# Kernel optimization log

Hardware: AMD Instinct MI355X
Metric: run time of the kernel (lower is better)

Reference implementation:

```python
import jax, jax.numpy as jnp
import numpy as np

BALL_SIZE = 128


def setup_inputs() -> dict:
    key = jax.random.key(0)
    kq, kk, kv = jax.random.split(key, 3)
    B, H, n, Dh = 4, 16, 8192, 64
    q = jax.random.normal(kq, (B, H, n, Dh), dtype=jnp.float32)
    k = jax.random.normal(kk, (B, H, n, Dh), dtype=jnp.float32)
    v = jax.random.normal(kv, (B, H, n, Dh), dtype=jnp.float32)
    return {"q": q, "k": k, "v": v}


def reference(q, k, v) -> jnp.ndarray:
    # Block-local (ball) attention: attention computed independently within
    # each contiguous ball of size BALL_SIZE along the sequence dim.
    B, H, n, Dh = q.shape
    bs = BALL_SIZE
    m = n // bs
    # (B, H, m, bs, D) -- split seq into balls; attention only within a ball.
    qb = q.reshape(B, H, m, bs, Dh)
    kb = k.reshape(B, H, m, bs, Dh)
    vb = v.reshape(B, H, m, bs, Dh)
    scale = 1.0 / jnp.sqrt(jnp.asarray(Dh, dtype=q.dtype))
    scores = jnp.einsum('bhmqd,bhmkd->bhmqk', qb, kb) * scale  # (B,H,m,bs,bs)
    attn = jax.nn.softmax(scores, axis=-1)
    out = jnp.einsum('bhmqk,bhmkd->bhmqd', attn, vb)
    return out.reshape(B, H, n, Dh)
```

## Files before the change

kernel.cpp:

```cpp
#include <hip/hip_runtime.h>

typedef _Float16 half2_t __attribute__((ext_vector_type(2)));
typedef _Float16 half4_t __attribute__((ext_vector_type(4)));
typedef _Float16 half8_t __attribute__((ext_vector_type(8)));
typedef __fp16   fp16x2  __attribute__((ext_vector_type(2)));
typedef float    f32x16  __attribute__((ext_vector_type(16)));

#define BS 128
#define DH 64

static __device__ __forceinline__ half2_t pkrtz(float x, float y) {
  fp16x2 t = __builtin_amdgcn_cvt_pkrtz(x, y);
  return __builtin_bit_cast(half2_t, t);
}
static __device__ __forceinline__ unsigned pkrtz_u(float x, float y) {
  fp16x2 t = __builtin_amdgcn_cvt_pkrtz(x, y);
  return __builtin_bit_cast(unsigned, t);
}

static __device__ __forceinline__ half8_t cvt8(const float4 a, const float4 b) {
  half2_t h0 = pkrtz(a.x, a.y);
  half2_t h1 = pkrtz(a.z, a.w);
  half2_t h2 = pkrtz(b.x, b.y);
  half2_t h3 = pkrtz(b.z, b.w);
  half4_t lo = __builtin_shufflevector(h0, h1, 0, 1, 2, 3);
  half4_t hi = __builtin_shufflevector(h2, h3, 0, 1, 2, 3);
  return __builtin_shufflevector(lo, hi, 0, 1, 2, 3, 4, 5, 6, 7);
}

static __device__ __forceinline__ half8_t h8_from(unsigned r0, unsigned r1,
                                                  unsigned r2, unsigned r3) {
  half2_t h0 = __builtin_bit_cast(half2_t, r0);
  half2_t h1 = __builtin_bit_cast(half2_t, r1);
  half2_t h2 = __builtin_bit_cast(half2_t, r2);
  half2_t h3 = __builtin_bit_cast(half2_t, r3);
  half4_t lo = __builtin_shufflevector(h0, h1, 0, 1, 2, 3);
  half4_t hi = __builtin_shufflevector(h2, h3, 0, 1, 2, 3);
  return __builtin_shufflevector(lo, hi, 0, 1, 2, 3, 4, 5, 6, 7);
}

static __device__ __forceinline__ void plswap(unsigned x, unsigned y,
                                              unsigned& olo, unsigned& ohi) {
#if __has_builtin(__builtin_amdgcn_permlane32_swap)
  auto pr = __builtin_amdgcn_permlane32_swap((int)x, (int)y, false, false);
  unsigned tmp[2];
  __builtin_memcpy(tmp, &pr, 8);
  olo = tmp[0];
  ohi = tmp[1];
#else
  const int h = (threadIdx.x & 63) >> 5;
  unsigned xs = (unsigned)__shfl_xor((int)x, 32);
  unsigned ys = (unsigned)__shfl_xor((int)y, 32);
  olo = h ? ys : x;
  ohi = h ? y : xs;
#endif
}

static __device__ __forceinline__ int svt(int d) { return (d & 7) ^ ((d >> 2) & 7); }

__global__ __launch_bounds__(256) void ball_attn_kernel(
    const float* __restrict__ Q, const float* __restrict__ Kk,
    const float* __restrict__ V, float* __restrict__ O) {
  __shared__ __align__(16) float    Kf[BS * DH];
  __shared__ __align__(16) _Float16 VT[DH * BS];

  const int tid  = threadIdx.x;
  const int w    = tid >> 6;
  const int lane = tid & 63;
  const int ld   = lane & 31;
  const int hi   = lane >> 5;

  const int nwg  = gridDim.x;
  const int bid  = blockIdx.x;
  const int ball = (bid & 7) * (nwg >> 3) + (bid >> 3);

  const size_t base = (size_t)ball * (BS * DH);
  const float* Qb = Q + base;
  const float* Kb = Kk + base;
  const float* Vb = V + base;
  float*       Ob = O + base;

  const int kgrp = tid >> 4;
  const int d0   = (tid & 15) * 4;
  const int qbase = 32 * w;

#pragma unroll
  for (int t = 0; t < 8; ++t) {
    const int r = 32 * w + 4 * t + (lane >> 4);
    const int u = (lane & 15) ^ (r & 15);
    __builtin_amdgcn_global_load_lds(
        (const __attribute__((address_space(1))) unsigned int*)(Kb + r * DH + u * 4),
        (__attribute__((address_space(3))) unsigned int*)&Kf[(32 * w + 4 * t) * DH],
        16, 0, 0);
  }
  float4 va[4], vb[4];
#pragma unroll
  for (int it = 0; it < 4; ++it) {
    const int keyA = 2 * kgrp + 32 * it;
    va[it] = *(const float4*)(Vb + (size_t)keyA * DH + d0);
    vb[it] = *(const float4*)(Vb + (size_t)(keyA + 1) * DH + d0);
  }
  float4 qa[4], qb[4];
#pragma unroll
  for (int ds = 0; ds < 4; ++ds) {
    const float* qp = Qb + (qbase + ld) * DH + ds * 16 + hi * 8;
    qa[ds] = *(const float4*)qp;
    qb[ds] = *(const float4*)(qp + 4);
  }
#pragma unroll
  for (int it = 0; it < 4; ++it) {
    const int keyA = 2 * kgrp + 32 * it;
    const float* ap = (const float*)&va[it];
    const float* bp = (const float*)&vb[it];
#pragma unroll
    for (int j = 0; j < 4; ++j) {
      const int d = d0 + j;
      *(half2_t*)&VT[d * BS + (keyA ^ (svt(d) << 3))] = pkrtz(ap[j], bp[j]);
    }
  }
  half8_t bq[4];
#pragma unroll
  for (int ds = 0; ds < 4; ++ds) bq[ds] = cvt8(qa[ds], qb[ds]);

  __syncthreads();

  f32x16 acc[4] = {};
  __builtin_amdgcn_s_setprio(1);
#pragma unroll
  for (int kt = 0; kt < 4; ++kt) {
    const int row = kt * 32 + ld;
    const int sr  = row & 15;
    const float* kr = &Kf[row * DH];
#pragma unroll
    for (int ds = 0; ds < 4; ++ds) {
      const int u0 = 4 * ds + 2 * hi;
      const float4 a = *(const float4*)&kr[(u0 ^ sr) * 4];
      const float4 b = *(const float4*)&kr[((u0 + 1) ^ sr) * 4];
      const half8_t ak = cvt8(a, b);
      acc[kt] = __builtin_amdgcn_mfma_f32_32x32x16_f16(ak, bq[ds], acc[kt], 0, 0, 0);
    }
  }
  __builtin_amdgcn_s_setprio(0);

  float sm = 0.f;
#pragma unroll
  for (int kt = 0; kt < 4; ++kt)
#pragma unroll
    for (int r = 0; r < 16; ++r) {
      const float p = __expf(acc[kt][r] * 0.125f);
      acc[kt][r] = p;
      sm += p;
    }
  sm += __shfl_xor(sm, 32);
  const float inv = __builtin_amdgcn_rcpf(sm);

  half8_t pf[8];
#pragma unroll
  for (int s = 0; s < 8; ++s) {
    const int kt = s >> 1;
    const int bA = 2 * (s & 1);
    const int bB = bA + 1;
    const unsigned A0 = pkrtz_u(acc[kt][4 * bA + 0] * inv, acc[kt][4 * bA + 1] * inv);
    const unsigned A1 = pkrtz_u(acc[kt][4 * bA + 2] * inv, acc[kt][4 * bA + 3] * inv);
    const unsigned B0 = pkrtz_u(acc[kt][4 * bB + 0] * inv, acc[kt][4 * bB + 1] * inv);
    const unsigned B1 = pkrtz_u(acc[kt][4 * bB + 2] * inv, acc[kt][4 * bB + 3] * inv);
    unsigned r0, r1, r2, r3;
    plswap(A0, B0, r0, r2);
    plswap(A1, B1, r1, r3);
    pf[s] = h8_from(r0, r1, r2, r3);
  }

  f32x16 o[2] = {};
  __builtin_amdgcn_s_setprio(1);
#pragma unroll
  for (int dt = 0; dt < 2; ++dt) {
    const int row = dt * 32 + ld;
    const int sv  = svt(row) << 3;
#pragma unroll
    for (int s = 0; s < 8; ++s) {
      const half8_t vf = *(const half8_t*)&VT[row * BS + ((16 * s + 8 * hi) ^ sv)];
      o[dt] = __builtin_amdgcn_mfma_f32_32x32x16_f16(pf[s], vf, o[dt], 0, 0, 0);
    }
  }
  __builtin_amdgcn_s_setprio(0);

#pragma unroll
  for (int dt = 0; dt < 2; ++dt)
#pragma unroll
    for (int r = 0; r < 16; ++r) {
      const int qrow = qbase + (r & 3) + 8 * (r >> 2) + 4 * hi;
      Ob[qrow * DH + dt * 32 + ld] = o[dt][r];
    }
}

extern "C" void kernel_launch(void* const* d_in, const int* in_sizes, int n_in,
                              void* d_out, int out_size, void* d_ws, size_t ws_size,
                              hipStream_t stream) {
  const float* q = (const float*)d_in[0];
  const float* k = (const float*)d_in[1];
  const float* v = (const float*)d_in[2];
  float* out = (float*)d_out;
  const int nballs = in_sizes[0] / (BS * DH);
  ball_attn_kernel<<<dim3(nballs), dim3(256), 0, stream>>>(q, k, v, out);
}
```

Measured before the change: 111.6 us.

## Stage K as fp16 in LDS and process two balls per 512-thread block

K is now loaded into registers, converted to fp16 once, and stored to a swizzled fp16 LDS tile, so each wave reads ready-made half8 fragments. This replaces the asynchronous global-to-LDS fp32 copy followed by conversion after each LDS read. Each workgroup now handles two balls with 512 threads and double-sized shared arrays, halving the grid. The cost is losing the async global_load_lds path, more registers held per thread, and a different occupancy profile.

```diff
diff --git a/kernel.cpp b/kernel.cpp
--- a/kernel.cpp
+++ b/kernel.cpp
@@ -16,6 +16,12 @@
 static __device__ __forceinline__ unsigned pkrtz_u(float x, float y) {
   fp16x2 t = __builtin_amdgcn_cvt_pkrtz(x, y);
   return __builtin_bit_cast(unsigned, t);
+}
+
+static __device__ __forceinline__ half4_t cvt4(const float4 a) {
+  half2_t h0 = pkrtz(a.x, a.y);
+  half2_t h1 = pkrtz(a.z, a.w);
+  return __builtin_shufflevector(h0, h1, 0, 1, 2, 3);
 }
 
 static __device__ __forceinline__ half8_t cvt8(const float4 a, const float4 b) {
@@ -58,55 +64,64 @@
 
 static __device__ __forceinline__ int svt(int d) { return (d & 7) ^ ((d >> 2) & 7); }
 
-__global__ __launch_bounds__(256) void ball_attn_kernel(
+__global__ __launch_bounds__(512) void ball_attn_kernel(
     const float* __restrict__ Q, const float* __restrict__ Kk,
     const float* __restrict__ V, float* __restrict__ O) {
-  __shared__ __align__(16) float    Kf[BS * DH];
-  __shared__ __align__(16) _Float16 VT[DH * BS];
+  __shared__ __align__(16) _Float16 KH[2][BS * DH];
+  __shared__ __align__(16) _Float16 VT[2][DH * BS];
 
   const int tid  = threadIdx.x;
-  const int w    = tid >> 6;
+  const int w8   = tid >> 6;
+  const int grp  = w8 >> 2;
+  const int w    = w8 & 3;
   const int lane = tid & 63;
   const int ld   = lane & 31;
   const int hi   = lane >> 5;
-
-  const int nwg  = gridDim.x;
-  const int bid  = blockIdx.x;
-  const int ball = (bid & 7) * (nwg >> 3) + (bid >> 3);
-
-  const size_t base = (size_t)ball * (BS * DH);
+  const int gtid = tid & 255;
+
+  const int nwg = gridDim.x;
+  const int bid = blockIdx.x;
+  const int blk = (bid & 7) * (nwg >> 3) + (bid >> 3);
+
+  const size_t base = ((size_t)blk * 2 + grp) * (BS * DH);
   const float* Qb = Q + base;
   const float* Kb = Kk + base;
   const float* Vb = V + base;
   float*       Ob = O + base;
-
-  const int kgrp = tid >> 4;
-  const int d0   = (tid & 15) * 4;
+  _Float16* kh = KH[grp];
+  _Float16* vt = VT[grp];
+
+  const int kgrp = gtid >> 4;
+  const int d0   = (gtid & 15) * 4;
   const int qbase = 32 * w;
 
-#pragma unroll
-  for (int t = 0; t < 8; ++t) {
-    const int r = 32 * w + 4 * t + (lane >> 4);
-    const int u = (lane & 15) ^ (r & 15);
-    __builtin_amdgcn_global_load_lds(
-        (const __attribute__((address_space(1))) unsigned int*)(Kb + r * DH + u * 4),
-        (__attribute__((address_space(3))) unsigned int*)&Kf[(32 * w + 4 * t) * DH],
-        16, 0, 0);
-  }
-  float4 va[4], vb[4];
+  float4 ka_[4], kb_[4], va[4], vb[4], qa[4], qb[4];
+#pragma unroll
+  for (int it = 0; it < 4; ++it) {
+    const int keyA = 2 * kgrp + 32 * it;
+    ka_[it] = *(const float4*)(Kb + (size_t)keyA * DH + d0);
+    kb_[it] = *(const float4*)(Kb + (size_t)(keyA + 1) * DH + d0);
+  }
 #pragma unroll
   for (int it = 0; it < 4; ++it) {
     const int keyA = 2 * kgrp + 32 * it;
     va[it] = *(const float4*)(Vb + (size_t)keyA * DH + d0);
     vb[it] = *(const float4*)(Vb + (size_t)(keyA + 1) * DH + d0);
   }
-  float4 qa[4], qb[4];
 #pragma unroll
   for (int ds = 0; ds < 4; ++ds) {
     const float* qp = Qb + (qbase + ld) * DH + ds * 16 + hi * 8;
     qa[ds] = *(const float4*)qp;
     qb[ds] = *(const float4*)(qp + 4);
   }
+
+#pragma unroll
+  for (int it = 0; it < 4; ++it) {
+    const int keyA = 2 * kgrp + 32 * it;
+    const int keyB = keyA + 1;
+    *(half4_t*)&kh[keyA * DH + (((d0 >> 3) ^ (keyA & 7)) * 8) + (d0 & 7)] = cvt4(ka_[it]);
+    *(half4_t*)&kh[keyB * DH + (((d0 >> 3) ^ (keyB & 7)) * 8) + (d0 & 7)] = cvt4(kb_[it]);
+  }
 #pragma unroll
   for (int it = 0; it < 4; ++it) {
     const int keyA = 2 * kgrp + 32 * it;
@@ -115,7 +130,7 @@
 #pragma unroll
     for (int j = 0; j < 4; ++j) {
       const int d = d0 + j;
-      *(half2_t*)&VT[d * BS + (keyA ^ (svt(d) << 3))] = pkrtz(ap[j], bp[j]);
+      *(half2_t*)&vt[d * BS + (keyA ^ (svt(d) << 3))] = pkrtz(ap[j], bp[j]);
     }
   }
   half8_t bq[4];
@@ -129,14 +144,12 @@
 #pragma unroll
   for (int kt = 0; kt < 4; ++kt) {
     const int row = kt * 32 + ld;
-    const int sr  = row & 15;
-    const float* kr = &Kf[row * DH];
+    const _Float16* kr = &kh[row * DH];
+    const int sr = row & 7;
 #pragma unroll
     for (int ds = 0; ds < 4; ++ds) {
-      const int u0 = 4 * ds + 2 * hi;
-      const float4 a = *(const float4*)&kr[(u0 ^ sr) * 4];
-      const float4 b = *(const float4*)&kr[((u0 + 1) ^ sr) * 4];
-      const half8_t ak = cvt8(a, b);
+      const int u = (2 * ds + hi) ^ sr;
+      const half8_t ak = *(const half8_t*)&kr[u * 8];
       acc[kt] = __builtin_amdgcn_mfma_f32_32x32x16_f16(ak, bq[ds], acc[kt], 0, 0, 0);
     }
   }
@@ -178,7 +191,7 @@
     const int sv  = svt(row) << 3;
 #pragma unroll
     for (int s = 0; s < 8; ++s) {
-      const half8_t vf = *(const half8_t*)&VT[row * BS + ((16 * s + 8 * hi) ^ sv)];
+      const half8_t vf = *(const half8_t*)&vt[row * BS + ((16 * s + 8 * hi) ^ sv)];
       o[dt] = __builtin_amdgcn_mfma_f32_32x32x16_f16(pf[s], vf, o[dt], 0, 0, 0);
     }
   }
@@ -201,5 +214,5 @@
   const float* v = (const float*)d_in[2];
   float* out = (float*)d_out;
   const int nballs = in_sizes[0] / (BS * DH);
-  ball_attn_kernel<<<dim3(nballs), dim3(256), 0, stream>>>(q, k, v, out);
-}
+  ball_attn_kernel<<<dim3(nballs / 2), dim3(512), 0, stream>>>(q, k, v, out);
+}
```

New measurement: 109.1 us. -2.2%, faster.
